# Performance work log

Measured on AMD Instinct MI355X. Metric: run time of the kernel, lower is better.

## Reference

```python
import jax, jax.numpy as jnp
import numpy as np
from jax import lax

B, C, H, W = 2, 64, 48, 48
NH, DK, DV = 8, 64, 128          # heads, per-head d_k, per-head d_v
DN, NS, R = 128, 16, 4           # SS2D d_inner (expand=2), d_state, dt_rank
MULT = 4                          # FFN expansion
L = H * W


def layer_norm(x, w, b, eps=1e-5):
    m = x.mean(-1, keepdims=True)
    v = ((x - m) ** 2).mean(-1, keepdims=True)
    return (x - m) / jnp.sqrt(v + eps) * w + b


def conv2d(x, w, groups=1):
    # x: NCHW, w: OIHW
    return lax.conv_general_dilated(x, w, (1, 1), 'SAME',
                                    dimension_numbers=('NCHW', 'OIHW', 'NCHW'),
                                    feature_group_count=groups)


def setup_inputs() -> dict:
    key = jax.random.key(0)
    ks = jax.random.split(key, 24)
    rn = lambda k, shp, s=0.02: jax.random.normal(k, shp, jnp.float32) * s
    inp = {
        'enc_input': jax.random.normal(ks[0], (B, C, H, W), jnp.float32),
        'slf_attn_snr': jax.random.uniform(ks[1], (B, 1, H, W), jnp.float32),
        # MultiHeadAttention params
        'attn_wq': rn(ks[2], (C, NH * DK)),
        'attn_wk': rn(ks[3], (C, NH * DK)),
        'attn_wv': rn(ks[4], (C, NH * DV)),
        'attn_fc': rn(ks[5], (NH * DV, C)),
        'attn_ln_w': jnp.ones((C,), jnp.float32),
        'attn_ln_b': jnp.zeros((C,), jnp.float32),
        # SS2D params
        'ss_in_w': rn(ks[6], (C, 2 * DN)),
        'ss_conv_w': rn(ks[7], (DN, 1, 3, 3)),
        'ss_conv_b': jnp.zeros((DN,), jnp.float32),
        'ss_xproj_w': rn(ks[8], (4, R + 2 * NS, DN)),
        'ss_dt_w': rn(ks[9], (4, DN, R)),
        'ss_dt_b': rn(ks[10], (4, DN)),
        'ss_Alog': jnp.log(jnp.broadcast_to(jnp.arange(1, NS + 1, dtype=jnp.float32), (4, DN, NS))),
        'ss_D': jnp.ones((4, DN), jnp.float32),
        'ss_norm_w': jnp.ones((DN,), jnp.float32),
        'ss_norm_b': jnp.zeros((DN,), jnp.float32),
        'ss_out_w': rn(ks[11], (DN, C)),
        # FFN (PreNorm + conv block)
        'ffn_ln_w': jnp.ones((C,), jnp.float32),
        'ffn_ln_b': jnp.zeros((C,), jnp.float32),
        'ffn_w1': rn(ks[12], (C * MULT, C, 1, 1)),
        'ffn_dw': rn(ks[13], (C * MULT, 1, 3, 3)),
        'ffn_w2': rn(ks[14], (C, C * MULT, 1, 1)),
    }
    return inp


def reference(enc_input, slf_attn_snr, attn_wq, attn_wk, attn_wv, attn_fc,
              attn_ln_w, attn_ln_b, ss_in_w, ss_conv_w, ss_conv_b, ss_xproj_w,
              ss_dt_w, ss_dt_b, ss_Alog, ss_D, ss_norm_w, ss_norm_b, ss_out_w,
              ffn_ln_w, ffn_ln_b, ffn_w1, ffn_dw, ffn_w2):
    # ---- Multi-head self-attention over spatial tokens (SNR-biased) ----
    x_tok = enc_input.reshape(B, C, L).transpose(0, 2, 1)        # (B, L, C)
    q = (x_tok @ attn_wq).reshape(B, L, NH, DK).transpose(0, 2, 1, 3)
    k = (x_tok @ attn_wk).reshape(B, L, NH, DK).transpose(0, 2, 1, 3)
    v = (x_tok @ attn_wv).reshape(B, L, NH, DV).transpose(0, 2, 1, 3)
    scores = jnp.einsum('bhqd,bhkd->bhqk', q, k) / jnp.sqrt(jnp.float32(DK))
    snr_flat = slf_attn_snr.reshape(B, 1, 1, L)                  # bias over keys
    scores = scores + jnp.log(snr_flat + 1e-4)
    attn = jax.nn.softmax(scores, axis=-1)                       # (B, NH, L, L)
    o = jnp.einsum('bhqk,bhkd->bhqd', attn, v)
    o = o.transpose(0, 2, 1, 3).reshape(B, L, NH * DV) @ attn_fc
    enc_output = layer_norm(o + x_tok, attn_ln_w, attn_ln_b)     # post-LN residual
    enc_output = enc_output.transpose(0, 2, 1).reshape(B, C, H, W)

    # ---- SS2D: 4-direction 2D selective scan ----
    xh = enc_output.transpose(0, 2, 3, 1)                        # (B, H, W, C)
    snr_h = slf_attn_snr.transpose(0, 2, 3, 1)                   # (B, H, W, 1)
    xz = xh @ ss_in_w                                            # (B, H, W, 2*DN)
    x1, z = xz[..., :DN], xz[..., DN:]
    x1 = x1.transpose(0, 3, 1, 2)                                # (B, DN, H, W)
    x1 = conv2d(x1, ss_conv_w, groups=DN) + ss_conv_b[None, :, None, None]
    x1 = jax.nn.silu(x1)

    x_hw = x1.reshape(B, DN, L)
    x_wh = x1.transpose(0, 1, 3, 2).reshape(B, DN, L)
    xs = jnp.stack([x_hw, x_wh], axis=1)                         # (B, 2, DN, L)
    xs = jnp.concatenate([xs, jnp.flip(xs, axis=-1)], axis=1)    # (B, 4, DN, L)

    x_dbl = jnp.einsum('bkdl,kcd->bkcl', xs, ss_xproj_w)
    dts, Bs, Cs = x_dbl[:, :, :R], x_dbl[:, :, R:R + NS], x_dbl[:, :, R + NS:]
    dts = jnp.einsum('bkrl,kdr->bkdl', dts, ss_dt_w) + ss_dt_b[None, :, :, None]
    dts = jax.nn.softplus(dts)                                   # (B, 4, DN, L)
    A = -jnp.exp(ss_Alog)                                        # (4, DN, NS)

    def step(h, inp):
        xt, dtt, Bt, Ct = inp                                    # (B,4,DN),(B,4,DN),(B,4,NS),(B,4,NS)
        dA = jnp.exp(dtt[..., None] * A)                         # (B,4,DN,NS)
        h = h * dA + (dtt * xt)[..., None] * Bt[:, :, None, :]
        y = jnp.einsum('bkdn,bkn->bkd', h, Ct)
        return h, y

    h0 = jnp.zeros((B, 4, DN, NS), jnp.float32)
    elems = (xs.transpose(3, 0, 1, 2), dts.transpose(3, 0, 1, 2),
             Bs.transpose(3, 0, 1, 2), Cs.transpose(3, 0, 1, 2))
    _, ys = lax.scan(step, h0, elems)                            # (L, B, 4, DN)
    ys = ys.transpose(1, 2, 3, 0) + ss_D[None, :, :, None] * xs  # (B, 4, DN, L)

    inv = jnp.flip(ys[:, 2:4], axis=-1)                          # undo reversed scans
    wh = ys[:, 1].reshape(B, DN, W, H).transpose(0, 1, 3, 2).reshape(B, DN, L)
    invwh = inv[:, 1].reshape(B, DN, W, H).transpose(0, 1, 3, 2).reshape(B, DN, L)
    y = ys[:, 0] + inv[:, 0] + wh + invwh                        # (B, DN, L)
    y = y.transpose(0, 2, 1).reshape(B, H, W, DN)
    y = layer_norm(y, ss_norm_w, ss_norm_b) * jax.nn.silu(z) * snr_h
    x2 = y @ ss_out_w + enc_input.transpose(0, 2, 3, 1)          # (B, H, W, C)

    # ---- PreNorm conv FeedForward ----
    xn = layer_norm(x2, ffn_ln_w, ffn_ln_b).transpose(0, 3, 1, 2)
    h1 = jax.nn.gelu(conv2d(xn, ffn_w1), approximate=False)
    h1 = jax.nn.gelu(conv2d(h1, ffn_dw, groups=C * MULT), approximate=False)
    h1 = conv2d(h1, ffn_w2).transpose(0, 2, 3, 1)
    x3 = h1 + x2

    return x3.transpose(0, 3, 1, 2)                              # (B, C, H, W)
```

## Files before the change

kernel.cpp:

```cpp
#include <hip/hip_runtime.h>
#include <hip/hip_bf16.h>

#define Bq 2
#define Cc 64
#define Hh 48
#define Ww 48
#define Ll 2304
#define NHh 8
#define DKk 64
#define DVv 128
#define DNn 128
#define NSs 16
#define Rr 4
#define SCH 48
#define SNC 48
#define TT 8

#define OQ    0u
#define OK_   2359296u
#define OV    4718592u
#define OO    9437184u
#define OX1P  14450688u
#define OZ    15040512u
#define OVT   15630336u
#define OLP   (OVT + 2359296u)
#define OX2   0u
#define WS_NEED_FLOATS (OVT + 4718592u)
#define ODT2  OQ
#define OYS2  OK_
#define OX1S  (OV + 1179648u)
#define OBS2  (OV + 1769472u)
#define OCS2  (OV + 2064384u)
#define OCSA  (OV + 2359296u)
#define OCSB  (OV + 3145728u)
#define OHST  (OV + 3932160u)
#define OH1A  OO
#define OH1B  (OO + 1179648u)

typedef short short8v __attribute__((ext_vector_type(8)));
typedef short short4v __attribute__((ext_vector_type(4)));
typedef float f32x4 __attribute__((ext_vector_type(4)));
typedef unsigned short ushort_t;

__device__ __forceinline__ float geluf(float x) {
  return 0.5f * x * (1.0f + erff(x * 0.70710678118654752f));
}
__device__ __forceinline__ float siluf(float x) {
  return x / (1.0f + __expf(-x));
}
__device__ __forceinline__ float softplusf(float x) {
  return fmaxf(x, 0.0f) + log1pf(__expf(-fabsf(x)));
}
__device__ __forceinline__ int spmap(int k, int l) {
  if (k == 0) return l;
  if (k == 1) return (l % 48) * 48 + l / 48;
  if (k == 2) return 2303 - l;
  int l2 = 2303 - l; return (l2 % 48) * 48 + l2 / 48;
}
__device__ __forceinline__ short f2bf(float f) {
  unsigned u = __float_as_uint(f);
  unsigned r = (u + 0x7FFFu + ((u >> 16) & 1u)) >> 16;
  return (short)r;
}

__global__ void k_code(float* out) { if (threadIdx.x == 0) out[0] = 25000.f; }

__global__ __launch_bounds__(256) void k_qkv(const float* __restrict__ enc,
    const float* __restrict__ wq, const float* __restrict__ wk,
    const float* __restrict__ wv, float* __restrict__ ws) {
  int l0 = blockIdx.x * TT; int b = blockIdx.y;
  int t = threadIdx.x;
  __shared__ float xs[64][12];
  {
    int idx = t, c = idx >> 3, i = idx & 7;
    xs[c][i] = enc[(size_t)b * Cc * Ll + (size_t)c * Ll + l0 + i];
    idx = t + 256; c = idx >> 3; i = idx & 7;
    xs[c][i] = enc[(size_t)b * Cc * Ll + (size_t)c * Ll + l0 + i];
  }
  __syncthreads();
  ushort_t* qb = (ushort_t*)(ws + OQ);
  ushort_t* kb = (ushort_t*)(ws + OK_);
  float* v = ws + OV;
#pragma unroll
  for (int g = 0; g < 6; ++g) {
    int j = t + g * 256;
    float acc[TT];
#pragma unroll
    for (int i = 0; i < TT; ++i) acc[i] = 0.f;
    const float* wp; int col, stride;
    if (j < 512) { wp = wq + j; stride = 512; col = j; }
    else if (j < 1024) { wp = wk + (j - 512); stride = 512; col = j - 512; }
    else { wp = wv + (j - 1024); stride = 1024; col = j - 1024; }
    for (int c = 0; c < 64; ++c) {
      float w = wp[(size_t)c * stride];
      const float4* xc = (const float4*)&xs[c][0];
      float4 x0 = xc[0], x1 = xc[1];
      acc[0] += x0.x * w; acc[1] += x0.y * w;
      acc[2] += x0.z * w; acc[3] += x0.w * w;
      acc[4] += x1.x * w; acc[5] += x1.y * w;
      acc[6] += x1.z * w; acc[7] += x1.w * w;
    }
    if (j < 512) {
#pragma unroll
      for (int i = 0; i < TT; ++i)
        qb[((size_t)(b * 8 + (col >> 6)) * Ll + l0 + i) * 64 + (col & 63)] =
            (ushort_t)f2bf(acc[i] * 0.125f);
    } else if (j < 1024) {
#pragma unroll
      for (int i = 0; i < TT; ++i)
        kb[((size_t)(b * 8 + (col >> 6)) * Ll + l0 + i) * 64 + (col & 63)] =
            (ushort_t)f2bf(acc[i]);
    } else {
#pragma unroll
      for (int i = 0; i < TT; ++i)
        v[((size_t)(b * 8 + (col >> 7)) * Ll + l0 + i) * 128 + (col & 127)] = acc[i];
    }
  }
}

__global__ __launch_bounds__(256) void k_vt(float* __restrict__ ws) {
  int bh = blockIdx.y;
  int l0 = blockIdx.x * 64;
  int t = threadIdx.x;
  __shared__ float tile[128][65];
  const float* vp = ws + OV + ((size_t)bh * Ll + l0) * 128;
  for (int i = t; i < 64 * 32; i += 256) {
    int l = i >> 5, dv4 = (i & 31) * 4;
    float4 a = *(const float4*)(vp + (size_t)l * 128 + dv4);
    tile[dv4][l] = a.x; tile[dv4 + 1][l] = a.y;
    tile[dv4 + 2][l] = a.z; tile[dv4 + 3][l] = a.w;
  }
  __syncthreads();
  ushort_t* vt = (ushort_t*)(ws + OVT) + (size_t)bh * 128 * Ll + l0;
  for (int i = t; i < 128 * 16; i += 256) {
    int dv = i >> 4, l4 = (i & 15) * 4;
    short4v a;
    a[0] = f2bf(tile[dv][l4]); a[1] = f2bf(tile[dv][l4 + 1]);
    a[2] = f2bf(tile[dv][l4 + 2]); a[3] = f2bf(tile[dv][l4 + 3]);
    *(short4v*)(vt + (size_t)dv * Ll + l4) = a;
  }
}

#define NKT2 18
#define LSK 72
__global__ __launch_bounds__(256) void k_attn(const float* __restrict__ snr,
                                              float* __restrict__ ws) {
  int bh = blockIdx.y; int b = bh >> 3; int hd = bh & 7;
  int q0 = blockIdx.x * 64;
  int ks = blockIdx.z;
  int kbase = ks * (Ll / 2);
  int t = threadIdx.x;
  int w = t >> 6, lane = t & 63;
  int m16 = lane & 15, quad = lane >> 4;

  __shared__ __align__(16) ushort_t Ks[64 * LSK];
  __shared__ __align__(16) ushort_t Vs[128 * LSK];
  __shared__ __align__(16) ushort_t Ps[4 * 16 * LSK];
  __shared__ float sfac_s[64];

  const ushort_t* qbf = (const ushort_t*)(ws + OQ) + (size_t)bh * Ll * 64;
  const ushort_t* kbf = (const ushort_t*)(ws + OK_) + (size_t)bh * Ll * 64;
  const ushort_t* vtb = (const ushort_t*)(ws + OVT) + (size_t)bh * 128 * Ll;

  short8v qa[2];
  {
    const ushort_t* qrp = qbf + (size_t)(q0 + w * 16 + m16) * 64 + quad * 8;
    qa[0] = *(const short8v*)qrp;
    qa[1] = *(const short8v*)(qrp + 32);
  }
  int sk_key = t >> 2, sk_d0 = (t & 3) * 16;
  int sv_dv = t >> 1, sv_k0 = (t & 1) * 32;

  short8v kreg[2], vreg[4];
  float snr_reg = 0.f;
  {
    const ushort_t* ksrc = kbf + (size_t)(kbase + sk_key) * 64 + sk_d0;
    kreg[0] = *(const short8v*)ksrc;
    kreg[1] = *(const short8v*)(ksrc + 8);
    const ushort_t* vsrc = vtb + (size_t)sv_dv * Ll + kbase + sv_k0;
#pragma unroll
    for (int i = 0; i < 4; ++i) vreg[i] = *(const short8v*)(vsrc + i * 8);
    if (t < 64) snr_reg = snr[b * Ll + kbase + t];
  }

  f32x4 oacc[8];
#pragma unroll
  for (int i = 0; i < 8; ++i) oacc[i] = (f32x4)0.f;
  float l_r[4] = {0.f, 0.f, 0.f, 0.f};

  for (int kt = 0; kt < NKT2; ++kt) {
    __syncthreads();
    *(short8v*)&Ks[sk_key * LSK + sk_d0] = kreg[0];
    *(short8v*)&Ks[sk_key * LSK + sk_d0 + 8] = kreg[1];
#pragma unroll
    for (int i = 0; i < 4; ++i)
      *(short8v*)&Vs[sv_dv * LSK + sv_k0 + i * 8] = vreg[i];
    if (t < 64) sfac_s[t] = snr_reg + 1e-4f;
    __syncthreads();
    if (kt + 1 < NKT2) {
      int k0n = kbase + (kt + 1) * 64;
      const ushort_t* ksrc = kbf + (size_t)(k0n + sk_key) * 64 + sk_d0;
      kreg[0] = *(const short8v*)ksrc;
      kreg[1] = *(const short8v*)(ksrc + 8);
      const ushort_t* vsrc = vtb + (size_t)sv_dv * Ll + k0n + sv_k0;
#pragma unroll
      for (int i = 0; i < 4; ++i) vreg[i] = *(const short8v*)(vsrc + i * 8);
      if (t < 64) snr_reg = snr[b * Ll + k0n + t];
    }

    f32x4 sac[4];
#pragma unroll
    for (int n = 0; n < 4; ++n) {
      int key = n * 16 + m16;
      short8v kb0 = *(const short8v*)&Ks[key * LSK + quad * 8];
      short8v kb1 = *(const short8v*)&Ks[key * LSK + 32 + quad * 8];
      f32x4 acc = (f32x4)0.f;
      acc = __builtin_amdgcn_mfma_f32_16x16x32_bf16(qa[0], kb0, acc, 0, 0, 0);
      acc = __builtin_amdgcn_mfma_f32_16x16x32_bf16(qa[1], kb1, acc, 0, 0, 0);
      sac[n] = acc;
    }
    float sf[4];
#pragma unroll
    for (int n = 0; n < 4; ++n) sf[n] = sfac_s[n * 16 + m16];
    ushort_t* pw = &Ps[w * 16 * LSK];
#pragma unroll
    for (int r = 0; r < 4; ++r) {
#pragma unroll
      for (int n = 0; n < 4; ++n) {
        float p = __expf(sac[n][r]) * sf[n];
        l_r[r] += p;
        pw[(quad * 4 + r) * LSK + n * 16 + m16] = (ushort_t)f2bf(p);
      }
    }
    short8v pb0 = *(const short8v*)&pw[m16 * LSK + quad * 8];
    short8v pb1 = *(const short8v*)&pw[m16 * LSK + 32 + quad * 8];
#pragma unroll
    for (int dt_ = 0; dt_ < 8; ++dt_) {
      const ushort_t* vrow = &Vs[(dt_ * 16 + m16) * LSK];
      short8v va0 = *(const short8v*)&vrow[quad * 8];
      short8v va1 = *(const short8v*)&vrow[32 + quad * 8];
      f32x4 o = oacc[dt_];
      o = __builtin_amdgcn_mfma_f32_16x16x32_bf16(va0, pb0, o, 0, 0, 0);
      o = __builtin_amdgcn_mfma_f32_16x16x32_bf16(va1, pb1, o, 0, 0, 0);
      oacc[dt_] = o;
    }
  }
#pragma unroll
  for (int r = 0; r < 4; ++r) {
    float lv = l_r[r];
    lv += __shfl_xor(lv, 1, 64);
    lv += __shfl_xor(lv, 2, 64);
    lv += __shfl_xor(lv, 4, 64);
    lv += __shfl_xor(lv, 8, 64);
    l_r[r] = lv;
  }
  if (m16 == 0) {
    float* lp = ws + OLP + (size_t)ks * (Bq * NHh * Ll) + (size_t)bh * Ll;
#pragma unroll
    for (int r = 0; r < 4; ++r) lp[q0 + w * 16 + quad * 4 + r] = l_r[r];
  }
  float* opb = ws + (ks ? OV : OO);
  float* op = opb + ((size_t)(b * Ll + q0 + w * 16 + m16)) * 1024 + hd * 128;
#pragma unroll
  for (int dt_ = 0; dt_ < 8; ++dt_) {
#pragma unroll
    for (int r = 0; r < 4; ++r) {
      op[dt_ * 16 + quad * 4 + r] = oacc[dt_][r];
    }
  }
}

__global__ __launch_bounds__(256) void k_oprojxz(const float* __restrict__ enc,
    const float* __restrict__ fc, const float* __restrict__ lnw,
    const float* __restrict__ lnb, const float* __restrict__ ssin,
    float* __restrict__ ws) {
  int l0 = blockIdx.x * TT, b = blockIdx.y, t = threadIdx.x;
  __shared__ float orow[1024][9];
  __shared__ float part[4][TT][64];
  __shared__ float xh_s[64][9];
  __shared__ float linv_s[8][TT];
  if (t < 64) {
    int hd = t >> 3, i = t & 7;
    float l1 = ws[OLP + (size_t)(b * 8 + hd) * Ll + l0 + i];
    float l2 = ws[OLP + (size_t)(Bq * NHh * Ll) + (size_t)(b * 8 + hd) * Ll + l0 + i];
    linv_s[hd][i] = 1.f / (l1 + l2);
  }
  __syncthreads();
  const float* op0 = ws + OO + ((size_t)(b * Ll + l0)) * 1024;
  const float* op1 = ws + OV + ((size_t)(b * Ll + l0)) * 1024;
#pragma unroll
  for (int k = 0; k < 4; ++k) {
    int c = t + k * 256;
    float li[TT];
#pragma unroll
    for (int i = 0; i < TT; ++i) li[i] = linv_s[c >> 7][i];
#pragma unroll
    for (int i = 0; i < TT; ++i)
      orow[c][i] = (op0[(size_t)i * 1024 + c] + op1[(size_t)i * 1024 + c]) * li[i];
  }
  __syncthreads();
  int col = t & 63, seg = t >> 6;
  {
    float acc[TT];
#pragma unroll
    for (int i = 0; i < TT; ++i) acc[i] = 0.f;
    const float* fcs = fc + (size_t)(seg * 256) * 64 + col;
    for (int c = 0; c < 256; ++c) {
      float w = fcs[(size_t)c * 64];
      const float* orc = &orow[seg * 256 + c][0];
#pragma unroll
      for (int i = 0; i < TT; ++i) acc[i] += orc[i] * w;
    }
#pragma unroll
    for (int i = 0; i < TT; ++i) part[seg][i][col] = acc[i];
  }
  __syncthreads();
  {
    float lw = lnw[col], lb = lnb[col];
#pragma unroll
    for (int i2 = 0; i2 < 2; ++i2) {
      int i = seg * 2 + i2;
      float a = part[0][i][col] + part[1][i][col] + part[2][i][col] + part[3][i][col];
      a += enc[(size_t)b * Cc * Ll + (size_t)col * Ll + l0 + i];
      float s = a;
#pragma unroll
      for (int o = 32; o >= 1; o >>= 1) s += __shfl_xor(s, o, 64);
      float m = s * (1.f / 64.f);
      float dd = a - m;
      float vs = dd * dd;
#pragma unroll
      for (int o = 32; o >= 1; o >>= 1) vs += __shfl_xor(vs, o, 64);
      xh_s[col][i] = dd * rsqrtf(vs * (1.f / 64.f) + 1e-5f) * lw + lb;
    }
  }
  __syncthreads();
  {
    float acc2[TT];
#pragma unroll
    for (int i = 0; i < TT; ++i) acc2[i] = 0.f;
    for (int c = 0; c < 64; ++c) {
      float w = ssin[c * 256 + t];
      const float* xc = &xh_s[c][0];
#pragma unroll
      for (int i = 0; i < TT; ++i) acc2[i] += xc[i] * w;
    }
    if (t < 128) {
#pragma unroll
      for (int i = 0; i < TT; ++i)
        ws[OX1P + ((size_t)(b * Ll + l0 + i)) * 128 + t] = acc2[i];
    } else {
#pragma unroll
      for (int i = 0; i < TT; ++i)
        ws[OZ + ((size_t)(b * Ll + l0 + i)) * 128 + (t - 128)] = acc2[i];
    }
  }
}

__global__ __launch_bounds__(256) void k_conv(const float* __restrict__ cw,
    const float* __restrict__ cb, float* __restrict__ ws) {
  int l0 = blockIdx.x * TT, b = blockIdx.y, t = threadIdx.x;
  int h = l0 / 48, w0 = l0 % 48;
  __shared__ float tile[3][10][128];
  for (int idx = t; idx < 3840; idx += 256) {
    int r = idx / 1280, rem = idx % 1280;
    int col = rem >> 7, d = rem & 127;
    int hh = h + r - 1, wx = w0 + col - 1;
    float v = 0.f;
    if (hh >= 0 && hh < 48 && wx >= 0 && wx < 48)
      v = ws[OX1P + ((size_t)(b * Ll + hh * 48 + wx)) * 128 + d];
    tile[r][col][d] = v;
  }
  __syncthreads();
  int d = t & 127, half = t >> 7;
  float cwr[9];
#pragma unroll
  for (int j = 0; j < 9; ++j) cwr[j] = cw[d * 9 + j];
  float cbv = cb[d];
#pragma unroll
  for (int j = 0; j < 4; ++j) {
    int i = half * 4 + j;
    float acc = cbv;
#pragma unroll
    for (int kh = 0; kh < 3; ++kh)
#pragma unroll
      for (int kw = 0; kw < 3; ++kw)
        acc += tile[kh][i + kw][d] * cwr[kh * 3 + kw];
    ws[OX1S + ((size_t)(b * Ll + l0 + i)) * 128 + d] = siluf(acc);
  }
}

__global__ __launch_bounds__(128) void k_xdbl(const float* __restrict__ xw,
    const float* __restrict__ dtw, const float* __restrict__ dtb,
    float* __restrict__ ws) {
  int l0 = blockIdx.x * TT;
  int by = blockIdx.y; int b = by >> 2; int k = by & 3;
  int t = threadIdx.x;
  __shared__ float xv[128][9];
  __shared__ float pr[36][TT];
#pragma unroll
  for (int i = 0; i < TT; ++i) {
    int sp = spmap(k, l0 + i);
    xv[t][i] = ws[OX1S + ((size_t)(b * Ll) + sp) * 128 + t];
  }
  __syncthreads();
  if (t < 36) {
    float s[TT];
#pragma unroll
    for (int i = 0; i < TT; ++i) s[i] = 0.f;
    const float* wp = xw + (size_t)(k * 36 + t) * 128;
    for (int d = 0; d < 128; ++d) {
      float w = wp[d];
      const float* xc = &xv[d][0];
#pragma unroll
      for (int i = 0; i < TT; ++i) s[i] += xc[i] * w;
    }
#pragma unroll
    for (int i = 0; i < TT; ++i) pr[t][i] = s[i];
  }
  __syncthreads();
  {
    int d = t;
    const float* wp = dtw + (size_t)(k * 128 + d) * 4;
    float w0 = wp[0], w1 = wp[1], w2 = wp[2], w3 = wp[3];
    float bb = dtb[k * 128 + d];
#pragma unroll
    for (int i = 0; i < TT; ++i) {
      float v = pr[0][i] * w0 + pr[1][i] * w1 + pr[2][i] * w2 + pr[3][i] * w3 + bb;
      ws[ODT2 + ((size_t)(by * Ll + l0 + i)) * 128 + d] = softplusf(v);
    }
  }
  if (t < 16) {
#pragma unroll
    for (int i = 0; i < TT; ++i)
      ws[OBS2 + ((size_t)(by * Ll + l0 + i)) * 16 + t] = pr[4 + t][i];
  } else if (t < 32) {
#pragma unroll
    for (int i = 0; i < TT; ++i)
      ws[OCS2 + ((size_t)(by * Ll + l0 + i)) * 16 + (t - 16)] = pr[20 + (t - 16)][i];
  }
}

__global__ __launch_bounds__(256) void k_scanA(const float* __restrict__ alog,
                                               float* __restrict__ ws) {
  int c = blockIdx.x;
  int bk = blockIdx.y;
  int b = bk >> 2, k = bk & 3;
  int t = threadIdx.x;
  int n = t & 15, dg = t >> 4;
  __shared__ float dt_s[2][128], x_s[2][128], Bs_s[2][16];
  float A_r[8], ap[8], bc[8];
#pragma unroll
  for (int i = 0; i < 8; ++i) {
    int d = dg * 8 + i;
    A_r[i] = -__expf(alog[(size_t)((k * 128 + d) * 16) + n]);
    ap[i] = 1.f; bc[i] = 0.f;
  }
  const float* dtp = ws + ODT2 + ((size_t)bk * Ll) * 128;
  const float* bsp = ws + OBS2 + ((size_t)bk * Ll) * 16;
  const float* xb = ws + OX1S + (size_t)b * Ll * 128;
  float r_a = 0.f, r_Bs = 0.f;
  {
    int l = c * SCH;
    int sp = spmap(k, l);
    if (t < 128) r_a = dtp[(size_t)l * 128 + t];
    else r_a = xb[(size_t)sp * 128 + (t - 128)];
    if (t < 16) r_Bs = bsp[(size_t)l * 16 + t];
  }
  for (int ll = 0; ll < SCH; ++ll) {
    int buf = ll & 1;
    if (t < 128) dt_s[buf][t] = r_a;
    else x_s[buf][t - 128] = r_a;
    if (t < 16) Bs_s[buf][t] = r_Bs;
    __syncthreads();
    if (ll + 1 < SCH) {
      int l2 = c * SCH + ll + 1;
      int sp2 = spmap(k, l2);
      if (t < 128) r_a = dtp[(size_t)l2 * 128 + t];
      else r_a = xb[(size_t)sp2 * 128 + (t - 128)];
      if (t < 16) r_Bs = bsp[(size_t)l2 * 16 + t];
    }
    float Bv = Bs_s[buf][n];
#pragma unroll
    for (int i = 0; i < 8; ++i) {
      int d = dg * 8 + i;
      float dtv = dt_s[buf][d];
      float a = __expf(dtv * A_r[i]);
      bc[i] = bc[i] * a + dtv * x_s[buf][d] * Bv;
      ap[i] *= a;
    }
  }
  float* csa = ws + OCSA + ((size_t)(bk * SNC + c) * 128) * 16;
  float* csb = ws + OCSB + ((size_t)(bk * SNC + c) * 128) * 16;
#pragma unroll
  for (int i = 0; i < 8; ++i) {
    int d = dg * 8 + i;
    csa[d * 16 + n] = ap[i];
    csb[d * 16 + n] = bc[i];
  }
}

__global__ __launch_bounds__(256) void k_scanB(float* __restrict__ ws) {
  int g = blockIdx.x * 256 + threadIdx.x;
  int bk = g >> 11;
  int dn = g & 2047;
  const float* csa = ws + OCSA;
  const float* csb = ws + OCSB;
  float* hst = ws + OHST;
  size_t base = (size_t)bk * SNC * 2048 + dn;
  float h = 0.f;
  float a = csa[base], bq = csb[base];
  for (int c = 0; c < SNC; ++c) {
    float na = 0.f, nb = 0.f;
    if (c + 1 < SNC) {
      size_t idx2 = base + (size_t)(c + 1) * 2048;
      na = csa[idx2]; nb = csb[idx2];
    }
    hst[base + (size_t)c * 2048] = h;
    h = a * h + bq;
    a = na; bq = nb;
  }
}

__global__ __launch_bounds__(256) void k_scanC(const float* __restrict__ alog,
    const float* __restrict__ Dp, float* __restrict__ ws) {
  int c = blockIdx.x, bk = blockIdx.y;
  int b = bk >> 2, k = bk & 3;
  int t = threadIdx.x;
  int n = t & 15, dg = t >> 4;
  __shared__ float dt_s[2][128], x_s[2][128], Bs_s[2][16], Cs_s[2][16];
  float A_r[8], h[8], Dv[8];
#pragma unroll
  for (int i = 0; i < 8; ++i) {
    int d = dg * 8 + i;
    A_r[i] = -__expf(alog[(size_t)((k * 128 + d) * 16) + n]);
    h[i] = ws[OHST + ((size_t)(bk * SNC + c) * 128 + d) * 16 + n];
    Dv[i] = Dp[k * 128 + d];
  }
  const float* dtp = ws + ODT2 + ((size_t)bk * Ll) * 128;
  const float* bsp = ws + OBS2 + ((size_t)bk * Ll) * 16;
  const float* csp = ws + OCS2 + ((size_t)bk * Ll) * 16;
  const float* xb = ws + OX1S + (size_t)b * Ll * 128;
  float* yp = ws + OYS2 + ((size_t)bk * Ll) * 128;
  float r_a = 0.f, r_bc = 0.f;
  {
    int l = c * SCH;
    int sp = spmap(k, l);
    if (t < 128) r_a = dtp[(size_t)l * 128 + t];
    else r_a = xb[(size_t)sp * 128 + (t - 128)];
    if (t < 16) r_bc = bsp[(size_t)l * 16 + t];
    else if (t < 32) r_bc = csp[(size_t)l * 16 + (t - 16)];
  }
  for (int ll = 0; ll < SCH; ++ll) {
    int buf = ll & 1;
    if (t < 128) dt_s[buf][t] = r_a;
    else x_s[buf][t - 128] = r_a;
    if (t < 16) Bs_s[buf][t] = r_bc;
    else if (t < 32) Cs_s[buf][t - 16] = r_bc;
    __syncthreads();
    if (ll + 1 < SCH) {
      int l2 = c * SCH + ll + 1;
      int sp2 = spmap(k, l2);
      if (t < 128) r_a = dtp[(size_t)l2 * 128 + t];
      else r_a = xb[(size_t)sp2 * 128 + (t - 128)];
      if (t < 16) r_bc = bsp[(size_t)l2 * 16 + t];
      else if (t < 32) r_bc = csp[(size_t)l2 * 16 + (t - 16)];
    }
    int l = c * SCH + ll;
    float Bv = Bs_s[buf][n], Cv = Cs_s[buf][n];
    float yacc[8];
#pragma unroll
    for (int i = 0; i < 8; ++i) {
      int d = dg * 8 + i;
      float dtv = dt_s[buf][d];
      float a = __expf(dtv * A_r[i]);
      h[i] = h[i] * a + dtv * x_s[buf][d] * Bv;
      yacc[i] = h[i] * Cv;
    }
#pragma unroll
    for (int i = 0; i < 8; ++i) {
      float yv = yacc[i];
      yv += __shfl_xor(yv, 1, 64);
      yv += __shfl_xor(yv, 2, 64);
      yv += __shfl_xor(yv, 4, 64);
      yv += __shfl_xor(yv, 8, 64);
      yacc[i] = yv;
    }
    if (n == 0) {
#pragma unroll
      for (int i = 0; i < 8; ++i) {
        int d = dg * 8 + i;
        yp[(size_t)l * 128 + d] = yacc[i] + Dv[i] * x_s[buf][d];
      }
    }
  }
}

__global__ __launch_bounds__(256) void k_combffn1(const float* __restrict__ enc,
    const float* __restrict__ nw, const float* __restrict__ nb,
    const float* __restrict__ snr, const float* __restrict__ ow,
    const float* __restrict__ lw, const float* __restrict__ lb,
    const float* __restrict__ w1, float* __restrict__ ws) {
  int l0 = blockIdx.x * TT, b = blockIdx.y, t = threadIdx.x;
  __shared__ float yr[128][9];
  __shared__ float redm[2][TT], redq[2][TT];
  __shared__ float part[2][TT][64];
  __shared__ float xn_s[64][9];
  int lane = t & 63, wid = (t >> 6) & 1;
  float v[TT], m[TT];
  if (t < 128) {
    int d = t;
    const float* ysb = ws + OYS2;
#pragma unroll
    for (int i = 0; i < TT; ++i) {
      int l = l0 + i;
      int hh = l / 48, wwp = l % 48;
      int lT = wwp * 48 + hh;
      v[i] = ysb[((size_t)(b * 4 + 0) * Ll + l) * 128 + d] +
             ysb[((size_t)(b * 4 + 2) * Ll + (2303 - l)) * 128 + d] +
             ysb[((size_t)(b * 4 + 1) * Ll + lT) * 128 + d] +
             ysb[((size_t)(b * 4 + 3) * Ll + (2303 - lT)) * 128 + d];
    }
    float s[TT];
#pragma unroll
    for (int i = 0; i < TT; ++i) s[i] = v[i];
#pragma unroll
    for (int o = 32; o >= 1; o >>= 1)
#pragma unroll
      for (int i = 0; i < TT; ++i) s[i] += __shfl_xor(s[i], o, 64);
    if (lane == 0) {
#pragma unroll
      for (int i = 0; i < TT; ++i) redm[wid][i] = s[i];
    }
  }
  __syncthreads();
  if (t < 128) {
    float q[TT];
#pragma unroll
    for (int i = 0; i < TT; ++i) {
      m[i] = (redm[0][i] + redm[1][i]) * (1.f / 128.f);
      float dv = v[i] - m[i];
      q[i] = dv * dv;
    }
#pragma unroll
    for (int o = 32; o >= 1; o >>= 1)
#pragma unroll
      for (int i = 0; i < TT; ++i) q[i] += __shfl_xor(q[i], o, 64);
    if (lane == 0) {
#pragma unroll
      for (int i = 0; i < TT; ++i) redq[wid][i] = q[i];
    }
  }
  __syncthreads();
  if (t < 128) {
    int d = t;
    float nwv = nw[d], nbv = nb[d];
#pragma unroll
    for (int i = 0; i < TT; ++i) {
      int l = l0 + i;
      float var = (redq[0][i] + redq[1][i]) * (1.f / 128.f);
      float y = (v[i] - m[i]) * rsqrtf(var + 1e-5f) * nwv + nbv;
      float zv = ws[OZ + ((size_t)(b * Ll + l)) * 128 + d];
      y *= siluf(zv);
      y *= snr[b * Ll + l];
      yr[d][i] = y;
    }
  }
  __syncthreads();
  if (t < 128) {
    int col = t & 63, seg = t >> 6;
    float acc[TT];
#pragma unroll
    for (int i = 0; i < TT; ++i) acc[i] = 0.f;
    const float* ows = ow + (size_t)(seg * 64) * 64 + col;
    for (int c = 0; c < 64; ++c) {
      float w = ows[c * 64];
      const float* yc = &yr[seg * 64 + c][0];
#pragma unroll
      for (int i = 0; i < TT; ++i) acc[i] += yc[i] * w;
    }
#pragma unroll
    for (int i = 0; i < TT; ++i) part[seg][i][col] = acc[i];
  }
  __syncthreads();
  {
    int wv = t >> 6, col2 = t & 63;
    float lwv = lw[col2], lbv = lb[col2];
#pragma unroll
    for (int i2 = 0; i2 < 2; ++i2) {
      int i = wv * 2 + i2;
      float a = part[0][i][col2] + part[1][i][col2];
      a += enc[(size_t)b * Cc * Ll + (size_t)col2 * Ll + l0 + i];
      ws[OX2 + ((size_t)(b * Ll + l0 + i)) * 64 + col2] = a;
      float s = a;
#pragma unroll
      for (int o = 32; o >= 1; o >>= 1) s += __shfl_xor(s, o, 64);
      float mm = s * (1.f / 64.f);
      float dd2 = a - mm;
      float vs = dd2 * dd2;
#pragma unroll
      for (int o = 32; o >= 1; o >>= 1) vs += __shfl_xor(vs, o, 64);
      xn_s[col2][i] = dd2 * rsqrtf(vs * (1.f / 64.f) + 1e-5f) * lwv + lbv;
    }
  }
  __syncthreads();
  {
    float acc2[TT];
#pragma unroll
    for (int i = 0; i < TT; ++i) acc2[i] = 0.f;
    const float* wp = w1 + (size_t)t * 64;
    for (int c = 0; c < 64; ++c) {
      float w = wp[c];
      const float* xc = &xn_s[c][0];
#pragma unroll
      for (int i = 0; i < TT; ++i) acc2[i] += xc[i] * w;
    }
#pragma unroll
    for (int i = 0; i < TT; ++i)
      ws[OH1A + ((size_t)(b * Ll + l0 + i)) * 256 + t] = geluf(acc2[i]);
  }
}

__global__ __launch_bounds__(256) void k_ffndw(const float* __restrict__ dww,
                                               float* __restrict__ ws) {
  int l0 = blockIdx.x * TT, b = blockIdx.y, t = threadIdx.x;
  int h = l0 / 48, w0 = l0 % 48;
  __shared__ float tile[3][10][256];
  for (int idx = t; idx < 7680; idx += 256) {
    int r = idx / 2560, rem = idx % 2560;
    int col = rem >> 8, ch = rem & 255;
    int hh = h + r - 1, wx = w0 + col - 1;
    float v = 0.f;
    if (hh >= 0 && hh < 48 && wx >= 0 && wx < 48)
      v = ws[OH1A + ((size_t)(b * Ll + hh * 48 + wx)) * 256 + ch];
    tile[r][col][ch] = v;
  }
  __syncthreads();
  float dwr[9];
#pragma unroll
  for (int j = 0; j < 9; ++j) dwr[j] = dww[t * 9 + j];
#pragma unroll
  for (int i = 0; i < TT; ++i) {
    float acc = 0.f;
#pragma unroll
    for (int kh = 0; kh < 3; ++kh)
#pragma unroll
      for (int kw = 0; kw < 3; ++kw)
        acc += tile[kh][i + kw][t] * dwr[kh * 3 + kw];
    ws[OH1B + ((size_t)(b * Ll + l0 + i)) * 256 + t] = geluf(acc);
  }
}

__global__ __launch_bounds__(256) void k_ffn2(const float* __restrict__ w2,
                                              float* __restrict__ ws,
                                              float* __restrict__ out) {
  int l0 = blockIdx.x * TT, b = blockIdx.y, t = threadIdx.x;
  __shared__ float hr[256][9];
  __shared__ float part[4][TT][64];
  const float* hp = ws + OH1B + ((size_t)(b * Ll + l0)) * 256;
#pragma unroll
  for (int i = 0; i < TT; ++i) hr[t][i] = hp[(size_t)i * 256 + t];
  __syncthreads();
  int col = t & 63, seg = t >> 6;
  {
    float acc[TT];
#pragma unroll
    for (int i = 0; i < TT; ++i) acc[i] = 0.f;
    const float* wp = w2 + (size_t)col * 256 + seg * 64;
    for (int c = 0; c < 64; ++c) {
      float w = wp[c];
      const float* hc = &hr[seg * 64 + c][0];
#pragma unroll
      for (int i = 0; i < TT; ++i) acc[i] += hc[i] * w;
    }
#pragma unroll
    for (int i = 0; i < TT; ++i) part[seg][i][col] = acc[i];
  }
  __syncthreads();
  if (t < 64) {
    float av[TT];
#pragma unroll
    for (int i = 0; i < TT; ++i) {
      float a = part[0][i][t] + part[1][i][t] + part[2][i][t] + part[3][i][t];
      av[i] = a + ws[OX2 + ((size_t)(b * Ll + l0 + i)) * 64 + t];
    }
    float* opx = out + ((size_t)(b * 64 + t)) * 2304 + l0;
    *(float4*)opx = make_float4(av[0], av[1], av[2], av[3]);
    *((float4*)opx + 1) = make_float4(av[4], av[5], av[6], av[7]);
  }
}

extern "C" void kernel_launch(void* const* d_in, const int* in_sizes, int n_in,
                              void* d_out, int out_size, void* d_ws, size_t ws_size,
                              hipStream_t stream) {
  (void)in_sizes; (void)n_in; (void)out_size;
  const float* enc  = (const float*)d_in[0];
  const float* snr  = (const float*)d_in[1];
  const float* wq   = (const float*)d_in[2];
  const float* wk   = (const float*)d_in[3];
  const float* wv   = (const float*)d_in[4];
  const float* fc   = (const float*)d_in[5];
  const float* alnw = (const float*)d_in[6];
  const float* alnb = (const float*)d_in[7];
  const float* ssin = (const float*)d_in[8];
  const float* cw   = (const float*)d_in[9];
  const float* cb   = (const float*)d_in[10];
  const float* xw   = (const float*)d_in[11];
  const float* dtw  = (const float*)d_in[12];
  const float* dtb  = (const float*)d_in[13];
  const float* alog = (const float*)d_in[14];
  const float* Dp   = (const float*)d_in[15];
  const float* nw   = (const float*)d_in[16];
  const float* nb   = (const float*)d_in[17];
  const float* ow   = (const float*)d_in[18];
  const float* flnw = (const float*)d_in[19];
  const float* flnb = (const float*)d_in[20];
  const float* w1   = (const float*)d_in[21];
  const float* dww  = (const float*)d_in[22];
  const float* w2   = (const float*)d_in[23];
  float* ws = (float*)d_ws;
  float* out = (float*)d_out;

  if (ws_size < (size_t)WS_NEED_FLOATS * 4) {
    hipLaunchKernelGGL(k_code, dim3(1), dim3(64), 0, stream, out);
    return;
  }

  hipLaunchKernelGGL(k_qkv, dim3(Ll / TT, Bq), dim3(256), 0, stream, enc, wq, wk, wv, ws);
  hipLaunchKernelGGL(k_vt, dim3(Ll / 64, Bq * NHh), dim3(256), 0, stream, ws);
  hipLaunchKernelGGL(k_attn, dim3(Ll / 64, Bq * NHh, 2), dim3(256), 0, stream, snr, ws);
  hipLaunchKernelGGL(k_oprojxz, dim3(Ll / TT, Bq), dim3(256), 0, stream, enc, fc, alnw, alnb, ssin, ws);
  hipLaunchKernelGGL(k_conv, dim3(Ll / TT, Bq), dim3(256), 0, stream, cw, cb, ws);
  hipLaunchKernelGGL(k_xdbl, dim3(Ll / TT, Bq * 4), dim3(128), 0, stream, xw, dtw, dtb, ws);
  hipLaunchKernelGGL(k_scanA, dim3(SNC, Bq * 4), dim3(256), 0, stream, alog, ws);
  hipLaunchKernelGGL(k_scanB, dim3(64), dim3(256), 0, stream, ws);
  hipLaunchKernelGGL(k_scanC, dim3(SNC, Bq * 4), dim3(256), 0, stream, alog, Dp, ws);
  hipLaunchKernelGGL(k_combffn1, dim3(Ll / TT, Bq), dim3(256), 0, stream, enc, nw, nb, snr, ow, flnw, flnb, w1, ws);
  hipLaunchKernelGGL(k_ffndw, dim3(Ll / TT, Bq), dim3(256), 0, stream, dww, ws);
  hipLaunchKernelGGL(k_ffn2, dim3(Ll / TT, Bq), dim3(256), 0, stream, w2, ws, out);
}
```

Baseline: 424.7 us.

## Store attention partials as bf16 and compute output projection with MFMA

The split-K attention kernel now writes its two partial outputs in bf16 instead of fp32, which halves that write and read traffic. A new small kernel pre-transposes the fc weight into bf16. The output projection then combines the partials, normalizes them into a bf16 LDS tile, and runs the 1024x64 projection with 16x16x32 bf16 MFMA over 16-token tiles instead of scalar FMA. Precision drops because partial sums and weights are rounded to bf16.

Result: faster. 415.0 us (-2.3%).

```diff
diff --git a/kernel.cpp b/kernel.cpp
--- a/kernel.cpp
+++ b/kernel.cpp
@@ -15,6 +15,7 @@
 #define SCH 48
 #define SNC 48
 #define TT 8
+#define TT2 16
 
 #define OQ    0u
 #define OK_   2359296u
@@ -24,6 +25,7 @@
 #define OZ    15040512u
 #define OVT   15630336u
 #define OLP   (OVT + 2359296u)
+#define OFCB  (OVT + 2433024u)
 #define OX2   0u
 #define WS_NEED_FLOATS (OVT + 4718592u)
 #define ODT2  OQ
@@ -61,6 +63,9 @@
   unsigned u = __float_as_uint(f);
   unsigned r = (u + 0x7FFFu + ((u >> 16) & 1u)) >> 16;
   return (short)r;
+}
+__device__ __forceinline__ float bfu2f(ushort_t u) {
+  return __uint_as_float(((unsigned)u) << 16);
 }
 
 __global__ void k_code(float* out) { if (threadIdx.x == 0) out[0] = 25000.f; }
@@ -141,6 +146,15 @@
   }
 }
 
+__global__ __launch_bounds__(256) void k_fcbf(const float* __restrict__ fc,
+                                              float* __restrict__ ws) {
+  int col = blockIdx.x;
+  int t = threadIdx.x;
+  ushort_t* dst = (ushort_t*)(ws + OFCB) + (size_t)col * 1024;
+  for (int k = t; k < 1024; k += 256)
+    dst[k] = (ushort_t)f2bf(fc[(size_t)k * 64 + col]);
+}
+
 #define NKT2 18
 #define LSK 72
 __global__ __launch_bounds__(256) void k_attn(const float* __restrict__ snr,
@@ -259,69 +273,68 @@
 #pragma unroll
     for (int r = 0; r < 4; ++r) lp[q0 + w * 16 + quad * 4 + r] = l_r[r];
   }
-  float* opb = ws + (ks ? OV : OO);
-  float* op = opb + ((size_t)(b * Ll + q0 + w * 16 + m16)) * 1024 + hd * 128;
+  ushort_t* opb = (ushort_t*)(ws + (ks ? OV : OO));
+  ushort_t* op = opb + ((size_t)(b * Ll + q0 + w * 16 + m16)) * 1024 + hd * 128;
 #pragma unroll
   for (int dt_ = 0; dt_ < 8; ++dt_) {
-#pragma unroll
-    for (int r = 0; r < 4; ++r) {
-      op[dt_ * 16 + quad * 4 + r] = oacc[dt_][r];
-    }
+    short4v o4;
+#pragma unroll
+    for (int r = 0; r < 4; ++r) o4[r] = f2bf(oacc[dt_][r]);
+    *(short4v*)&op[dt_ * 16 + quad * 4] = o4;
   }
 }
 
 __global__ __launch_bounds__(256) void k_oprojxz(const float* __restrict__ enc,
-    const float* __restrict__ fc, const float* __restrict__ lnw,
-    const float* __restrict__ lnb, const float* __restrict__ ssin,
-    float* __restrict__ ws) {
-  int l0 = blockIdx.x * TT, b = blockIdx.y, t = threadIdx.x;
-  __shared__ float orow[1024][9];
-  __shared__ float part[4][TT][64];
-  __shared__ float xh_s[64][9];
-  __shared__ float linv_s[8][TT];
-  if (t < 64) {
-    int hd = t >> 3, i = t & 7;
+    const float* __restrict__ lnw, const float* __restrict__ lnb,
+    const float* __restrict__ ssin, float* __restrict__ ws) {
+  int l0 = blockIdx.x * TT2, b = blockIdx.y, t = threadIdx.x;
+  int w = t >> 6, lane = t & 63, m16 = lane & 15, quad = lane >> 4;
+  __shared__ __align__(16) ushort_t obf[16][1040];
+  __shared__ float linv_s[8][16];
+  __shared__ float part[16][68];
+  __shared__ float xh_s[64][17];
+  if (t < 128) {
+    int hd = t >> 4, i = t & 15;
     float l1 = ws[OLP + (size_t)(b * 8 + hd) * Ll + l0 + i];
     float l2 = ws[OLP + (size_t)(Bq * NHh * Ll) + (size_t)(b * 8 + hd) * Ll + l0 + i];
     linv_s[hd][i] = 1.f / (l1 + l2);
   }
   __syncthreads();
-  const float* op0 = ws + OO + ((size_t)(b * Ll + l0)) * 1024;
-  const float* op1 = ws + OV + ((size_t)(b * Ll + l0)) * 1024;
-#pragma unroll
-  for (int k = 0; k < 4; ++k) {
-    int c = t + k * 256;
-    float li[TT];
-#pragma unroll
-    for (int i = 0; i < TT; ++i) li[i] = linv_s[c >> 7][i];
-#pragma unroll
-    for (int i = 0; i < TT; ++i)
-      orow[c][i] = (op0[(size_t)i * 1024 + c] + op1[(size_t)i * 1024 + c]) * li[i];
-  }
-  __syncthreads();
-  int col = t & 63, seg = t >> 6;
-  {
-    float acc[TT];
-#pragma unroll
-    for (int i = 0; i < TT; ++i) acc[i] = 0.f;
-    const float* fcs = fc + (size_t)(seg * 256) * 64 + col;
-    for (int c = 0; c < 256; ++c) {
-      float w = fcs[(size_t)c * 64];
-      const float* orc = &orow[seg * 256 + c][0];
-#pragma unroll
-      for (int i = 0; i < TT; ++i) acc[i] += orc[i] * w;
-    }
-#pragma unroll
-    for (int i = 0; i < TT; ++i) part[seg][i][col] = acc[i];
-  }
-  __syncthreads();
-  {
+  const ushort_t* p0 = (const ushort_t*)(ws + OO) + (size_t)(b * Ll + l0) * 1024;
+  const ushort_t* p1 = (const ushort_t*)(ws + OV) + (size_t)(b * Ll + l0) * 1024;
+#pragma unroll
+  for (int g = 0; g < 8; ++g) {
+    int v = t + g * 256;
+    int tok = v >> 7, k0 = (v & 127) * 8;
+    short8v a = *(const short8v*)(p0 + (size_t)tok * 1024 + k0);
+    short8v bb = *(const short8v*)(p1 + (size_t)tok * 1024 + k0);
+    float li = linv_s[k0 >> 7][tok];
+    short8v o;
+#pragma unroll
+    for (int j = 0; j < 8; ++j)
+      o[j] = f2bf((bfu2f((ushort_t)a[j]) + bfu2f((ushort_t)bb[j])) * li);
+    *(short8v*)&obf[tok][k0] = o;
+  }
+  __syncthreads();
+  f32x4 cacc = (f32x4)0.f;
+  const ushort_t* fcb = (const ushort_t*)(ws + OFCB) +
+                        (size_t)(w * 16 + m16) * 1024 + quad * 8;
+#pragma unroll
+  for (int kb = 0; kb < 32; ++kb) {
+    short8v a = *(const short8v*)&obf[m16][kb * 32 + quad * 8];
+    short8v bf = *(const short8v*)(fcb + kb * 32);
+    cacc = __builtin_amdgcn_mfma_f32_16x16x32_bf16(a, bf, cacc, 0, 0, 0);
+  }
+#pragma unroll
+  for (int r = 0; r < 4; ++r) part[quad * 4 + r][w * 16 + m16] = cacc[r];
+  __syncthreads();
+  {
+    int col = lane;
     float lw = lnw[col], lb = lnb[col];
 #pragma unroll
-    for (int i2 = 0; i2 < 2; ++i2) {
-      int i = seg * 2 + i2;
-      float a = part[0][i][col] + part[1][i][col] + part[2][i][col] + part[3][i][col];
-      a += enc[(size_t)b * Cc * Ll + (size_t)col * Ll + l0 + i];
+    for (int i2 = 0; i2 < 4; ++i2) {
+      int i = w * 4 + i2;
+      float a = part[i][col] + enc[(size_t)b * Cc * Ll + (size_t)col * Ll + l0 + i];
       float s = a;
 #pragma unroll
       for (int o = 32; o >= 1; o >>= 1) s += __shfl_xor(s, o, 64);
@@ -335,22 +348,22 @@
   }
   __syncthreads();
   {
-    float acc2[TT];
-#pragma unroll
-    for (int i = 0; i < TT; ++i) acc2[i] = 0.f;
+    float acc2[TT2];
+#pragma unroll
+    for (int i = 0; i < TT2; ++i) acc2[i] = 0.f;
     for (int c = 0; c < 64; ++c) {
-      float w = ssin[c * 256 + t];
+      float wv_ = ssin[c * 256 + t];
       const float* xc = &xh_s[c][0];
 #pragma unroll
-      for (int i = 0; i < TT; ++i) acc2[i] += xc[i] * w;
+      for (int i = 0; i < TT2; ++i) acc2[i] += xc[i] * wv_;
     }
     if (t < 128) {
 #pragma unroll
-      for (int i = 0; i < TT; ++i)
+      for (int i = 0; i < TT2; ++i)
         ws[OX1P + ((size_t)(b * Ll + l0 + i)) * 128 + t] = acc2[i];
     } else {
 #pragma unroll
-      for (int i = 0; i < TT; ++i)
+      for (int i = 0; i < TT2; ++i)
         ws[OZ + ((size_t)(b * Ll + l0 + i)) * 128 + (t - 128)] = acc2[i];
     }
   }
@@ -827,8 +840,9 @@
 
   hipLaunchKernelGGL(k_qkv, dim3(Ll / TT, Bq), dim3(256), 0, stream, enc, wq, wk, wv, ws);
   hipLaunchKernelGGL(k_vt, dim3(Ll / 64, Bq * NHh), dim3(256), 0, stream, ws);
+  hipLaunchKernelGGL(k_fcbf, dim3(64), dim3(256), 0, stream, fc, ws);
   hipLaunchKernelGGL(k_attn, dim3(Ll / 64, Bq * NHh, 2), dim3(256), 0, stream, snr, ws);
-  hipLaunchKernelGGL(k_oprojxz, dim3(Ll / TT, Bq), dim3(256), 0, stream, enc, fc, alnw, alnb, ssin, ws);
+  hipLaunchKernelGGL(k_oprojxz, dim3(Ll / TT2, Bq), dim3(256), 0, stream, enc, alnw, alnb, ssin, ws);
   hipLaunchKernelGGL(k_conv, dim3(Ll / TT, Bq), dim3(256), 0, stream, cw, cb, ws);
   hipLaunchKernelGGL(k_xdbl, dim3(Ll / TT, Bq * 4), dim3(128), 0, stream, xw, dtw, dtb, ws);
   hipLaunchKernelGGL(k_scanA, dim3(SNC, Bq * 4), dim3(256), 0, stream, alog, ws);
```
